# Optimization experiments

Measured on AMD Instinct MI355X. Metric: run time of the kernel, lower is better.

The kernel has to match this reference:

```python
import jax, jax.numpy as jnp
import numpy as np

NEG_INF = -jnp.inf


def _forward(q, k, v, q_indexer, k_indexer, weights, index_topk, end_pos):
    b, h, s, d = q.shape
    scale = float(1.0 / np.sqrt(d))

    # ---- bf16_index: per-head relu(qk) weighted-sum over indexer heads ----
    qi = jnp.swapaxes(q_indexer, 1, 2).astype(jnp.float32)        # [b,hi,s,di]
    ki = jnp.transpose(k_indexer, (0, 2, 3, 1)).astype(jnp.float32)  # [b,hk,di,s] (hk=1 broadcasts)
    p = jax.nn.relu(jnp.matmul(qi, ki))                            # [b,hi,s,s]
    index_score = jnp.einsum('bhqk,bqh->bqk', p, weights.astype(jnp.float32))  # [b,s,s]

    # ---- causal additive mask (attn_mask=None path) ----
    causal = jnp.where(jnp.triu(jnp.ones((s, s), bool), 1), NEG_INF, 0.0).astype(jnp.float32)
    index_score = index_score + causal[None]

    # ---- top-k sparse index selection ----
    K = min(int(index_topk), int(end_pos))
    topk_score, topk_idx = jax.lax.top_k(index_score, K)           # [b,s,K]
    qpos = jnp.arange(s)[None, :, None]
    valid = topk_idx <= qpos
    # invalid slots: torch writes -1 (wraps to last col on CUDA); last col is causally
    # masked for those rows, so dropping the scatter gives an identical final mask.
    scatter_idx = jnp.where(valid, topk_idx, s)
    index_mask = jnp.full((b, s, s), NEG_INF).at[
        jnp.arange(b)[:, None, None], jnp.arange(s)[None, :, None], scatter_idx
    ].set(0.0, mode='drop')

    am = causal[None] + index_mask                                 # [b,s,s]
    masked = jnp.isinf(am) & (am < 0)                              # True = masked out
    keep = ~masked[:, None]                                        # [b,1,s,s]

    # ---- sparse SDPA ----
    scores = jnp.einsum('bhqd,bhkd->bhqk', q, k) * scale
    scores = jnp.where(keep, scores, NEG_INF)
    attn = jax.nn.softmax(scores.astype(jnp.float32), axis=-1)     # [b,h,s,s]
    output = jnp.einsum('bhqk,bhkd->bhqd', attn.astype(q.dtype), v)

    # ---- indexer auxiliary loss (main attn dist uses detached q,k) ----
    main_attn_dist = jax.lax.stop_gradient(attn).sum(axis=1)       # [b,s,s]
    gather_idx = jnp.where(valid, topk_idx, s - 1)                 # -1 wraps to last col
    sel = jnp.take_along_axis(main_attn_dist, gather_idx, axis=-1) # [b,s,K]
    pdist = jax.nn.softmax(topk_score.astype(jnp.float32), axis=-1)
    tgt = sel / jnp.maximum(jnp.sum(jnp.abs(sel), axis=-1, keepdims=True), 1e-12)
    # F.kl_div(log(p+eps), tgt+eps): t*(log t - log p)
    kl = (tgt + 1e-8) * (jnp.log(tgt + 1e-8) - jnp.log(pdist + 1e-8))
    loss = kl.sum(-1).mean()
    return loss, output


def setup_inputs() -> dict:
    key = jax.random.key(0)
    ks = jax.random.split(key, 6)
    b, h, s, d = 1, 16, 2048, 128
    hi, di = 16, 128
    return {
        'q': jax.random.normal(ks[0], (b, h, s, d), jnp.float32),
        'k': jax.random.normal(ks[1], (b, h, s, d), jnp.float32),
        'v': jax.random.normal(ks[2], (b, h, s, d), jnp.float32),
        'q_indexer': jax.random.normal(ks[3], (b, s, hi, di), jnp.float32),
        'k_indexer': jax.random.normal(ks[4], (b, s, 1, di), jnp.float32),
        'weights': jax.random.uniform(ks[5], (b, s, hi), jnp.float32),
        'index_topk': 512,
        'end_pos': 2048,
    }


def reference(q, k, v, q_indexer, k_indexer, weights, index_topk, end_pos):
    return _forward(q, k, v, q_indexer, k_indexer, weights, index_topk, end_pos)
```

## Files before the change

kernel.cpp:

```cpp
#include <hip/hip_runtime.h>
#include <hip/hip_bf16.h>
#include <hip/hip_fp16.h>
#include <math.h>

#define S    2048
#define HQ   16
#define D    128
#define HI   16
#define DI   128
#define KSEL 512
#define OPW  132

typedef __attribute__((ext_vector_type(8))) short short8;
typedef __attribute__((ext_vector_type(4))) float f32x4;
typedef __attribute__((ext_vector_type(2))) float f32x2;
typedef __attribute__((ext_vector_type(2))) _Float16 h2v;

__device__ __forceinline__ float waveReduceSum(float v) {
#pragma unroll
    for (int o = 32; o > 0; o >>= 1) v += __shfl_down(v, o);
    return v;
}
__device__ __forceinline__ float waveReduceMax(float v) {
#pragma unroll
    for (int o = 32; o > 0; o >>= 1) v = fmaxf(v, __shfl_down(v, o));
    return v;
}
__device__ __forceinline__ float blockReduceSum(float v, float* tmp) {
    int wid = threadIdx.x >> 6, lane = threadIdx.x & 63;
    v = waveReduceSum(v);
    __syncthreads();
    if (lane == 0) tmp[wid] = v;
    __syncthreads();
    return tmp[0] + tmp[1] + tmp[2] + tmp[3];
}
__device__ __forceinline__ float blockReduceMax(float v, float* tmp) {
    int wid = threadIdx.x >> 6, lane = threadIdx.x & 63;
    v = waveReduceMax(v);
    __syncthreads();
    if (lane == 0) tmp[wid] = v;
    __syncthreads();
    return fmaxf(fmaxf(tmp[0], tmp[1]), fmaxf(tmp[2], tmp[3]));
}

__device__ __forceinline__ unsigned short f2bf(float f) {
    unsigned int u = __float_as_uint(f);
    return (unsigned short)((u + 0x7FFFu + ((u >> 16) & 1u)) >> 16);
}
__device__ __forceinline__ float bf2f(unsigned short h) {
    return __uint_as_float(((unsigned int)h) << 16);
}
__device__ __forceinline__ float fdot2u(unsigned int a, unsigned int b, float c) {
    return __builtin_amdgcn_fdot2(__builtin_bit_cast(h2v, a),
                                  __builtin_bit_cast(h2v, b), c, false);
}
__device__ __forceinline__ f32x2 f2shfl_xor(f32x2 v, int m) {
    f32x2 r;
    r.x = __shfl_xor(v.x, m);
    r.y = __shfl_xor(v.y, m);
    return r;
}

__global__ __launch_bounds__(256) void f32_to_f16(const float* __restrict__ in,
                                                  unsigned short* __restrict__ outp,
                                                  int n4) {
    for (int i = blockIdx.x * 256 + threadIdx.x; i < n4; i += gridDim.x * 256) {
        float4 x = ((const float4*)in)[i];
        uint2 r;
        r.x = __builtin_bit_cast(unsigned int, __floats2half2_rn(x.x, x.y));
        r.y = __builtin_bit_cast(unsigned int, __floats2half2_rn(x.z, x.w));
        ((uint2*)outp)[i] = r;
    }
}

__global__ __launch_bounds__(256) void f32_to_fp8(const float* __restrict__ in,
                                                  unsigned int* __restrict__ outp,
                                                  int n4) {
    for (int i = blockIdx.x * 256 + threadIdx.x; i < n4; i += gridDim.x * 256) {
        float4 x = ((const float4*)in)[i];
        int u = 0;
        u = __builtin_amdgcn_cvt_pk_fp8_f32(x.x, x.y, u, false);
        u = __builtin_amdgcn_cvt_pk_fp8_f32(x.z, x.w, u, true);
        outp[i] = (unsigned int)u;
    }
}

__global__ __launch_bounds__(256) void split_f32_bf16(const float* __restrict__ in,
                                                      unsigned short* __restrict__ hi,
                                                      unsigned short* __restrict__ lo,
                                                      int n4) {
    for (int i = blockIdx.x * 256 + threadIdx.x; i < n4; i += gridDim.x * 256) {
        float4 x = ((const float4*)in)[i];
        ushort4 h4, l4;
        h4.x = f2bf(x.x); l4.x = f2bf(x.x - bf2f(h4.x));
        h4.y = f2bf(x.y); l4.y = f2bf(x.y - bf2f(h4.y));
        h4.z = f2bf(x.z); l4.z = f2bf(x.z - bf2f(h4.z));
        h4.w = f2bf(x.w); l4.w = f2bf(x.w - bf2f(h4.w));
        ((ushort4*)hi)[i] = h4;
        ((ushort4*)lo)[i] = l4;
    }
}

__device__ void topk_from_scores(const float* scores, int ncand, int K, int q,
                                 int* __restrict__ topk_idx, float* __restrict__ topk_score,
                                 unsigned int* bins, unsigned int* sh_u, unsigned int* cnt_p) {
    const int tid = threadIdx.x;
    if (ncand <= K) {
        for (int j = tid; j < KSEL; j += 256) {
            if (j < ncand) {
                topk_idx[q * KSEL + j]   = j;
                topk_score[q * KSEL + j] = scores[j];
            } else {
                topk_idx[q * KSEL + j]   = -1;
                topk_score[q * KSEL + j] = -INFINITY;
            }
        }
        __syncthreads();
        return;
    }

    unsigned int prefix = 0;
    int need = K;
    for (int pass = 0; pass < 4; ++pass) {
        const int shift = 24 - pass * 8;
        for (int b = tid; b < 256; b += 256) bins[b] = 0;
        __syncthreads();
        const unsigned int himask = (pass == 0) ? 0u : (0xFFFFFFFFu << (shift + 8));
        for (int k = tid; k < ncand; k += 256) {
            unsigned int u = __float_as_uint(scores[k]);
            if ((u & himask) == prefix) atomicAdd(&bins[(u >> shift) & 0xFF], 1u);
        }
        __syncthreads();
        if (tid == 0) {
            int nd = need, b;
            for (b = 255; b >= 1; --b) {
                int c = (int)bins[b];
                if (c >= nd) break;
                nd -= c;
            }
            sh_u[0] = prefix | ((unsigned int)b << shift);
            sh_u[1] = (unsigned int)nd;
        }
        __syncthreads();
        prefix = sh_u[0];
        need   = (int)sh_u[1];
        __syncthreads();
    }
    const unsigned int ueqT = prefix;
    const int count_eq = (int)bins[ueqT & 0xFF];
    __syncthreads();
    if (tid == 0) *cnt_p = 0;
    __syncthreads();

    for (int k = tid; k < ncand; k += 256) {
        unsigned int u = __float_as_uint(scores[k]);
        if (u > ueqT) {
            unsigned int slot = atomicAdd(cnt_p, 1u);
            topk_idx[q * KSEL + slot]   = k;
            topk_score[q * KSEL + slot] = scores[k];
        }
    }
    __syncthreads();
    if (count_eq == need) {
        for (int k = tid; k < ncand; k += 256) {
            if (__float_as_uint(scores[k]) == ueqT) {
                unsigned int slot = atomicAdd(cnt_p, 1u);
                topk_idx[q * KSEL + slot]   = k;
                topk_score[q * KSEL + slot] = __uint_as_float(ueqT);
            }
        }
    } else if (tid == 0) {
        int emitted = 0;
        for (int k = 0; k < ncand && emitted < need; ++k) {
            if (__float_as_uint(scores[k]) == ueqT) {
                unsigned int slot = atomicAdd(cnt_p, 1u);
                topk_idx[q * KSEL + slot]   = k;
                topk_score[q * KSEL + slot] = __uint_as_float(ueqT);
                emitted++;
            }
        }
    }
    __syncthreads();
}

__global__ __launch_bounds__(256) void indexer_mfma(
    const unsigned short* __restrict__ qih, const unsigned short* __restrict__ qil,
    const unsigned short* __restrict__ kih, const unsigned short* __restrict__ kil,
    const float* __restrict__ w,
    const int* __restrict__ topk_p, const int* __restrict__ endpos_p,
    int* __restrict__ topk_idx, float* __restrict__ topk_score)
{
    const int tid  = threadIdx.x;
    const int wv   = tid >> 6;
    const int lane = tid & 63;
    int K = min(topk_p[0], endpos_p[0]);
    K = min(K, KSEL);

    __shared__ float scores[S];
    __shared__ float w_sh[HI];
    __shared__ unsigned int bins[256];
    __shared__ unsigned int sh_u[3];
    __shared__ unsigned int cnt;

    const int mrow = lane & 15;
    const int kgrp = lane >> 4;

    const int b = blockIdx.x;
    for (int qq = 0; qq < 2; ++qq) {
        const int q = qq ? (S - 1 - b) : b;
        if (tid < HI) w_sh[tid] = w[q * HI + tid];
        __syncthreads();

        short8 Ah[4], Al[4];
        {
            const unsigned short* bh = qih + ((size_t)q * HI + mrow) * DI + kgrp * 8;
            const unsigned short* bl = qil + ((size_t)q * HI + mrow) * DI + kgrp * 8;
#pragma unroll
            for (int dc = 0; dc < 4; dc++) {
                Ah[dc] = *(const short8*)(bh + dc * 32);
                Al[dc] = *(const short8*)(bl + dc * 32);
            }
        }
        float wreg[4];
#pragma unroll
        for (int e = 0; e < 4; e++) wreg[e] = w_sh[4 * kgrp + e];

        const int nkt = (q >> 4) + 1;
        for (int t = wv; t < nkt; t += 4) {
            const int k0 = t * 16;
            const unsigned short* bh = kih + ((size_t)(k0 + mrow)) * DI + kgrp * 8;
            const unsigned short* bl = kil + ((size_t)(k0 + mrow)) * DI + kgrp * 8;
            f32x4 acc = {0.f, 0.f, 0.f, 0.f};
#pragma unroll
            for (int dc = 0; dc < 4; dc++) {
                short8 Bh = *(const short8*)(bh + dc * 32);
                short8 Bl = *(const short8*)(bl + dc * 32);
                acc = __builtin_amdgcn_mfma_f32_16x16x32_bf16(Ah[dc], Bh, acc, 0, 0, 0);
                acc = __builtin_amdgcn_mfma_f32_16x16x32_bf16(Ah[dc], Bl, acc, 0, 0, 0);
                acc = __builtin_amdgcn_mfma_f32_16x16x32_bf16(Al[dc], Bh, acc, 0, 0, 0);
            }
            float part = wreg[0] * fmaxf(acc[0], 0.f) + wreg[1] * fmaxf(acc[1], 0.f)
                       + wreg[2] * fmaxf(acc[2], 0.f) + wreg[3] * fmaxf(acc[3], 0.f);
            part += __shfl_xor(part, 16);
            part += __shfl_xor(part, 32);
            if (lane < 16) {
                int k = k0 + lane;
                if (k <= q) scores[k] = part;
            }
        }
        __syncthreads();
        topk_from_scores(scores, q + 1, K, q, topk_idx, topk_score, bins, sh_u, &cnt);
    }
}

__global__ __launch_bounds__(256) void indexer_topk(
    const float* __restrict__ qi,
    const float* __restrict__ ki,
    const float* __restrict__ w,
    const int* __restrict__ topk_p, const int* __restrict__ endpos_p,
    int* __restrict__ topk_idx,
    float* __restrict__ topk_score)
{
    const int q   = blockIdx.x;
    const int tid = threadIdx.x;
    int K = min(topk_p[0], endpos_p[0]);
    K = min(K, KSEL);

    __shared__ float qis[HI * DI];
    __shared__ float wsh[HI];
    __shared__ float scores[S];
    __shared__ unsigned int bins[256];
    __shared__ unsigned int sh_u[3];
    __shared__ unsigned int cnt;

    for (int i = tid; i < HI * DI; i += 256) qis[i] = qi[(size_t)q * HI * DI + i];
    if (tid < HI) wsh[tid] = w[q * HI + tid];
    __syncthreads();

    const int ncand = q + 1;

    for (int kbase = 0; kbase < ncand; kbase += 1024) {
        const int k0 = kbase + tid * 4;
        if (k0 < ncand) {
            float acc[4][HI];
#pragma unroll
            for (int a = 0; a < 4; a++)
#pragma unroll
                for (int h = 0; h < HI; h++) acc[a][h] = 0.f;
            for (int d0 = 0; d0 < DI; d0 += 4) {
                float4 kv[4];
#pragma unroll
                for (int a = 0; a < 4; a++)
                    kv[a] = *(const float4*)&ki[(size_t)(k0 + a) * DI + d0];
#pragma unroll
                for (int h = 0; h < HI; h++) {
                    float4 qv = *(const float4*)&qis[h * DI + d0];
#pragma unroll
                    for (int a = 0; a < 4; a++) {
                        acc[a][h] += qv.x * kv[a].x + qv.y * kv[a].y +
                                     qv.z * kv[a].z + qv.w * kv[a].w;
                    }
                }
            }
#pragma unroll
            for (int a = 0; a < 4; a++) {
                int k = k0 + a;
                if (k < ncand) {
                    float s = 0.f;
#pragma unroll
                    for (int h = 0; h < HI; h++) s += wsh[h] * fmaxf(acc[a][h], 0.f);
                    scores[k] = s;
                }
            }
        }
    }
    __syncthreads();
    topk_from_scores(scores, ncand, K, q, topk_idx, topk_score, bins, sh_u, &cnt);
}

__global__ __launch_bounds__(256) void sparse_attn_v7(
    const float* __restrict__ Q,
    const unsigned short* __restrict__ Kh,
    const unsigned char* __restrict__ Vq,
    const int* __restrict__ topk_idx,
    const int* __restrict__ topk_p, const int* __restrict__ endpos_p,
    float* __restrict__ out,
    float* __restrict__ aacc_g)
{
    const int q   = blockIdx.x;
    const int h   = blockIdx.y;
    const int tid = threadIdx.x;
    int K = min(topk_p[0], endpos_p[0]);
    K = min(K, KSEL);
    const int n = min(q + 1, K);
    const float scale = 0.08838834764831845f;

    __shared__ int          offs[KSEL];
    __shared__ float        sc[KSEL];
    __shared__ unsigned int qh_u[64];
    __shared__ float        opart[16][OPW];
    __shared__ float        tmp[4];

    if (tid < 32) {
        float4 f = ((const float4*)&Q[((size_t)h * S + q) * D])[tid];
        qh_u[2 * tid]     = __builtin_bit_cast(unsigned int,
                              __floats2half2_rn(f.x * scale, f.y * scale));
        qh_u[2 * tid + 1] = __builtin_bit_cast(unsigned int,
                              __floats2half2_rn(f.z * scale, f.w * scale));
    }
    for (int j = tid; j < n; j += 256) offs[j] = topk_idx[q * KSEL + j] << 8;
    __syncthreads();

    const int l8 = tid & 7, grp8 = tid >> 3;
    unsigned int qa[4], qb[4];
#pragma unroll
    for (int c = 0; c < 4; c++) {
        qa[c] = qh_u[l8 * 4 + c];
        qb[c] = qh_u[32 + l8 * 4 + c];
    }
    const char* kbase = (const char*)Kh + (size_t)h * S * 256;
    for (int j = grp8; j < n; j += 32) {
        const char* rb = kbase + offs[j];
        uint4 ra  = *(const uint4*)(rb + l8 * 16);
        uint4 rb2 = *(const uint4*)(rb + 128 + l8 * 16);
        float acc0 = fdot2u(ra.x, qa[0], 0.f);
        float acc1 = fdot2u(rb2.x, qb[0], 0.f);
        acc0 = fdot2u(ra.y, qa[1], acc0);
        acc1 = fdot2u(rb2.y, qb[1], acc1);
        acc0 = fdot2u(ra.z, qa[2], acc0);
        acc1 = fdot2u(rb2.z, qb[2], acc1);
        acc0 = fdot2u(ra.w, qa[3], acc0);
        acc1 = fdot2u(rb2.w, qb[3], acc1);
        float acc = acc0 + acc1;
        acc += __shfl_xor(acc, 1);
        acc += __shfl_xor(acc, 2);
        acc += __shfl_xor(acc, 4);
        if (l8 == 0) sc[j] = acc;
    }
    __syncthreads();

    float lsum = 0.f;
    for (int j = tid; j < n; j += 256) {
        float p = __expf(sc[j]);
        sc[j] = p;
        lsum += p;
    }
    lsum = blockReduceSum(lsum, tmp);
    const float inv = 1.f / lsum;
    for (int j = tid; j < n; j += 256)
        atomicAdd(&aacc_g[(size_t)q * KSEL + j], sc[j] * inv);

    const char* vbase = (const char*)Vq + (size_t)h * S * 128;
    f32x2 o2[8];
#pragma unroll
    for (int i = 0; i < 8; i++) o2[i] = (f32x2){0.f, 0.f};
    for (int j = grp8; j < n; j += 32) {
        const float p = sc[j];
        const f32x2 p2 = {p, p};
        uint4 raw = *(const uint4*)(vbase + (offs[j] >> 1) + l8 * 16);
        o2[0] += p2 * __builtin_amdgcn_cvt_pk_f32_fp8((int)raw.x, false);
        o2[1] += p2 * __builtin_amdgcn_cvt_pk_f32_fp8((int)raw.x, true);
        o2[2] += p2 * __builtin_amdgcn_cvt_pk_f32_fp8((int)raw.y, false);
        o2[3] += p2 * __builtin_amdgcn_cvt_pk_f32_fp8((int)raw.y, true);
        o2[4] += p2 * __builtin_amdgcn_cvt_pk_f32_fp8((int)raw.z, false);
        o2[5] += p2 * __builtin_amdgcn_cvt_pk_f32_fp8((int)raw.z, true);
        o2[6] += p2 * __builtin_amdgcn_cvt_pk_f32_fp8((int)raw.w, false);
        o2[7] += p2 * __builtin_amdgcn_cvt_pk_f32_fp8((int)raw.w, true);
    }
#pragma unroll
    for (int i = 0; i < 8; i++) o2[i] += f2shfl_xor(o2[i], 32);
    const int lane = tid & 63, wvi = tid >> 6;
    if (lane < 32) {
        const int row = wvi * 4 + (lane >> 3);
        float* dst = &opart[row][(lane & 7) * 16];
#pragma unroll
        for (int i = 0; i < 8; i += 2) {
            float4 s;
            s.x = o2[i].x;     s.y = o2[i].y;
            s.z = o2[i + 1].x; s.w = o2[i + 1].y;
            *(float4*)&dst[i * 2] = s;
        }
    }
    __syncthreads();
    if (tid < D) {
        float s = 0.f;
#pragma unroll
        for (int p16 = 0; p16 < 16; ++p16) s += opart[p16][tid];
        out[((size_t)h * S + q) * D + tid] = s * inv;
    }
}

__global__ __launch_bounds__(256) void sparse_attn2(
    const float* __restrict__ Q,
    const float* __restrict__ Km,
    const float* __restrict__ V,
    const int* __restrict__ topk_idx,
    const int* __restrict__ topk_p, const int* __restrict__ endpos_p,
    float* __restrict__ out,
    float* __restrict__ aacc_g)
{
    const int q   = blockIdx.x;
    const int h   = blockIdx.y;
    const int tid = threadIdx.x;
    int K = min(topk_p[0], endpos_p[0]);
    K = min(K, KSEL);
    const int n = min(q + 1, K);
    const float scale = 0.08838834764831845f;

    __shared__ float qvec[D];
    __shared__ int   idxs[KSEL];
    __shared__ float sc[KSEL];
    __shared__ float opart[8][D];
    __shared__ float tmp[4];

    if (tid < 32)
        *(float4*)&qvec[tid * 4] = *(const float4*)&Q[((size_t)h * S + q) * D + tid * 4];
    for (int j = tid; j < n; j += 256) idxs[j] = topk_idx[q * KSEL + j];
    __syncthreads();

    const int l16 = tid & 15, grp = tid >> 4;
    const float4 q1 = *(const float4*)&qvec[l16 * 4];
    const float4 q2 = *(const float4*)&qvec[64 + l16 * 4];
    float lmax = -INFINITY;
    for (int j = grp; j < n; j += 16) {
        const float* kr = &Km[((size_t)h * S + idxs[j]) * D];
        float4 k1 = *(const float4*)&kr[l16 * 4];
        float4 k2 = *(const float4*)&kr[64 + l16 * 4];
        float acc = q1.x * k1.x + q1.y * k1.y + q1.z * k1.z + q1.w * k1.w
                  + q2.x * k2.x + q2.y * k2.y + q2.z * k2.z + q2.w * k2.w;
        acc += __shfl_xor(acc, 1);
        acc += __shfl_xor(acc, 2);
        acc += __shfl_xor(acc, 4);
        acc += __shfl_xor(acc, 8);
        float s = acc * scale;
        if (l16 == 0) sc[j] = s;
        lmax = fmaxf(lmax, s);
    }
    const float m = blockReduceMax(lmax, tmp);

    float lsum = 0.f;
    for (int j = tid; j < n; j += 256) {
        float p = expf(sc[j] - m);
        sc[j] = p;
        lsum += p;
    }
    lsum = blockReduceSum(lsum, tmp);
    const float inv = 1.f / lsum;
    for (int j = tid; j < n; j += 256) {
        float p = sc[j] * inv;
        sc[j] = p;
        atomicAdd(&aacc_g[(size_t)q * KSEL + j], p);
    }
    __syncthreads();

    const int jg = tid >> 5, lD = (tid & 31) * 4;
    float4 o4 = make_float4(0.f, 0.f, 0.f, 0.f);
    for (int j = jg; j < n; j += 8) {
        const float p = sc[j];
        float4 vv = *(const float4*)&V[((size_t)h * S + idxs[j]) * D + lD];
        o4.x += p * vv.x; o4.y += p * vv.y; o4.z += p * vv.z; o4.w += p * vv.w;
    }
    *(float4*)&opart[jg][lD] = o4;
    __syncthreads();
    if (tid < D) {
        float o = 0.f;
#pragma unroll
        for (int p8 = 0; p8 < 8; ++p8) o += opart[p8][tid];
        out[((size_t)h * S + q) * D + tid] = o;
    }
}

__global__ __launch_bounds__(256) void row_loss(
    const float* __restrict__ aacc_g,
    const float* __restrict__ topk_score,
    const int* __restrict__ topk_p, const int* __restrict__ endpos_p,
    float* __restrict__ rowloss)
{
    const int q   = blockIdx.x;
    const int tid = threadIdx.x;
    int K = min(topk_p[0], endpos_p[0]);
    K = min(K, KSEL);
    const int n = min(q + 1, K);

    __shared__ float sc[KSEL];
    __shared__ float aacc[KSEL];
    __shared__ float tmp[4];

    for (int j = tid; j < n; j += 256) aacc[j] = aacc_g[(size_t)q * KSEL + j];

    float tmaxl = -INFINITY;
    for (int j = tid; j < n; j += 256) {
        float t = topk_score[q * KSEL + j];
        sc[j] = t;
        tmaxl = fmaxf(tmaxl, t);
    }
    const float tm = blockReduceMax(tmaxl, tmp);
    float tsum = 0.f;
    for (int j = tid; j < n; j += 256) {
        float e = __expf(sc[j] - tm);
        sc[j] = e;
        tsum += e;
    }
    tsum = blockReduceSum(tsum, tmp);
    const float tinv = 1.f / tsum;

    float sa = 0.f;
    for (int j = tid; j < n; j += 256) sa += fabsf(aacc[j]);
    sa = blockReduceSum(sa, tmp);
    const float denom = fmaxf(sa, 1e-12f);

    float kl = 0.f;
    for (int j = tid; j < n; j += 256) {
        float tgt = aacc[j] / denom + 1e-8f;
        float pd  = sc[j] * tinv + 1e-8f;
        kl += tgt * (logf(tgt) - logf(pd));
    }
    kl = blockReduceSum(kl, tmp);
    if (tid == 0) rowloss[q] = kl;
}

__global__ __launch_bounds__(256) void reduce_loss(const float* __restrict__ rowloss,
                                                   float* __restrict__ out) {
    __shared__ float tmp[4];
    float v = 0.f;
    for (int i = threadIdx.x; i < S; i += 256) v += rowloss[i];
    v = blockReduceSum(v, tmp);
    if (threadIdx.x == 0) out[0] = v / (float)S;
}

extern "C" void kernel_launch(void* const* d_in, const int* in_sizes, int n_in,
                              void* d_out, int out_size, void* d_ws, size_t ws_size,
                              hipStream_t stream) {
    const float* q   = (const float*)d_in[0];
    const float* k   = (const float*)d_in[1];
    const float* v   = (const float*)d_in[2];
    const float* qi  = (const float*)d_in[3];
    const float* ki  = (const float*)d_in[4];
    const float* w   = (const float*)d_in[5];
    const int* topk  = (const int*)d_in[6];
    const int* endp  = (const int*)d_in[7];
    float* out = (float*)d_out;

    char* ws = (char*)d_ws;
    const size_t MB = 1ull << 20;
    int*   topk_idx   = (int*)ws;
    float* topk_score = (float*)(ws + 4 * MB);
    float* aacc_g     = (float*)(ws + 8 * MB);
    float* rowloss    = (float*)(ws + 12 * MB);
    char*  pbuf       = ws + 12 * MB + 65536;
    unsigned short* Kh  = (unsigned short*)pbuf;
    unsigned char*  Vq  = (unsigned char*)(pbuf + 8 * MB);
    unsigned short* qih = (unsigned short*)(pbuf + 12 * MB);
    unsigned short* qil = (unsigned short*)(pbuf + 20 * MB);
    unsigned short* kih = (unsigned short*)(pbuf + 28 * MB);
    unsigned short* kil = (unsigned short*)(pbuf + 28 * MB + 512 * 1024);
    const size_t need_attn = 12 * MB + 65536 + 12 * MB;
    const size_t need_idx  = 12 * MB + 65536 + 29 * MB;

    if (ws_size >= need_idx) {
        hipLaunchKernelGGL(split_f32_bf16, dim3(2048), dim3(256), 0, stream,
                           qi, qih, qil, S * HI * DI / 4);
        hipLaunchKernelGGL(split_f32_bf16, dim3(256), dim3(256), 0, stream,
                           ki, kih, kil, S * DI / 4);
        hipLaunchKernelGGL(indexer_mfma, dim3(S / 2), dim3(256), 0, stream,
                           qih, qil, kih, kil, w, topk, endp, topk_idx, topk_score);
    } else {
        hipLaunchKernelGGL(indexer_topk, dim3(S), dim3(256), 0, stream,
                           qi, ki, w, topk, endp, topk_idx, topk_score);
    }

    hipMemsetAsync(aacc_g, 0, (size_t)S * KSEL * sizeof(float), stream);

    if (ws_size >= need_attn) {
        const int n4 = HQ * S * D / 4;
        hipLaunchKernelGGL(f32_to_f16, dim3(2048), dim3(256), 0, stream, k, Kh, n4);
        hipLaunchKernelGGL(f32_to_fp8, dim3(2048), dim3(256), 0, stream, v,
                           (unsigned int*)Vq, n4);
        hipLaunchKernelGGL(sparse_attn_v7, dim3(S, HQ), dim3(256), 0, stream,
                           q, Kh, Vq, topk_idx, topk, endp, out + 1, aacc_g);
    } else {
        hipLaunchKernelGGL(sparse_attn2, dim3(S, HQ), dim3(256), 0, stream,
                           q, k, v, topk_idx, topk, endp, out + 1, aacc_g);
    }

    hipLaunchKernelGGL(row_loss, dim3(S), dim3(256), 0, stream,
                       aacc_g, topk_score, topk, endp, rowloss);
    hipLaunchKernelGGL(reduce_loss, dim3(1), dim3(256), 0, stream,
                       rowloss, out);
}
```

Baseline: 446.9 us.

## Fuse conversion kernels, parallelize radix-select bin scan, use fast log

Merges the two K/V conversion kernels into one launch and the two indexer split kernels into one launch, cutting launch overhead and inter-kernel gaps. Replaces the serial single-thread 256-bin threshold search in the top-k radix select with a 64-lane wave suffix-scan, shortening the critical path on every pass. Switches logf to __logf in the KL loss, trading a little accuracy for speed. The wave scan's boundary handling is more intricate, so tie and edge cases could behave differently from the serial loop.

```diff
diff --git a/kernel.cpp b/kernel.cpp
--- a/kernel.cpp
+++ b/kernel.cpp
@@ -61,44 +61,47 @@
     return r;
 }
 
-__global__ __launch_bounds__(256) void f32_to_f16(const float* __restrict__ in,
-                                                  unsigned short* __restrict__ outp,
+__global__ __launch_bounds__(256) void convert_kv(const float* __restrict__ kin,
+                                                  const float* __restrict__ vin,
+                                                  unsigned short* __restrict__ Kh,
+                                                  unsigned int* __restrict__ Vq,
                                                   int n4) {
-    for (int i = blockIdx.x * 256 + threadIdx.x; i < n4; i += gridDim.x * 256) {
-        float4 x = ((const float4*)in)[i];
+    const int stride = gridDim.x * 256;
+    for (int i = blockIdx.x * 256 + threadIdx.x; i < n4; i += stride) {
+        float4 x = ((const float4*)kin)[i];
         uint2 r;
         r.x = __builtin_bit_cast(unsigned int, __floats2half2_rn(x.x, x.y));
         r.y = __builtin_bit_cast(unsigned int, __floats2half2_rn(x.z, x.w));
-        ((uint2*)outp)[i] = r;
-    }
-}
-
-__global__ __launch_bounds__(256) void f32_to_fp8(const float* __restrict__ in,
-                                                  unsigned int* __restrict__ outp,
-                                                  int n4) {
-    for (int i = blockIdx.x * 256 + threadIdx.x; i < n4; i += gridDim.x * 256) {
-        float4 x = ((const float4*)in)[i];
+        ((uint2*)Kh)[i] = r;
+        float4 y = ((const float4*)vin)[i];
         int u = 0;
-        u = __builtin_amdgcn_cvt_pk_fp8_f32(x.x, x.y, u, false);
-        u = __builtin_amdgcn_cvt_pk_fp8_f32(x.z, x.w, u, true);
-        outp[i] = (unsigned int)u;
-    }
-}
-
-__global__ __launch_bounds__(256) void split_f32_bf16(const float* __restrict__ in,
-                                                      unsigned short* __restrict__ hi,
-                                                      unsigned short* __restrict__ lo,
-                                                      int n4) {
-    for (int i = blockIdx.x * 256 + threadIdx.x; i < n4; i += gridDim.x * 256) {
-        float4 x = ((const float4*)in)[i];
-        ushort4 h4, l4;
-        h4.x = f2bf(x.x); l4.x = f2bf(x.x - bf2f(h4.x));
-        h4.y = f2bf(x.y); l4.y = f2bf(x.y - bf2f(h4.y));
-        h4.z = f2bf(x.z); l4.z = f2bf(x.z - bf2f(h4.z));
-        h4.w = f2bf(x.w); l4.w = f2bf(x.w - bf2f(h4.w));
-        ((ushort4*)hi)[i] = h4;
-        ((ushort4*)lo)[i] = l4;
-    }
+        u = __builtin_amdgcn_cvt_pk_fp8_f32(y.x, y.y, u, false);
+        u = __builtin_amdgcn_cvt_pk_fp8_f32(y.z, y.w, u, true);
+        Vq[i] = (unsigned int)u;
+    }
+}
+
+__device__ __forceinline__ void split4(const float* in, unsigned short* hi,
+                                       unsigned short* lo, int i) {
+    float4 x = ((const float4*)in)[i];
+    ushort4 h4, l4;
+    h4.x = f2bf(x.x); l4.x = f2bf(x.x - bf2f(h4.x));
+    h4.y = f2bf(x.y); l4.y = f2bf(x.y - bf2f(h4.y));
+    h4.z = f2bf(x.z); l4.z = f2bf(x.z - bf2f(h4.z));
+    h4.w = f2bf(x.w); l4.w = f2bf(x.w - bf2f(h4.w));
+    ((ushort4*)hi)[i] = h4;
+    ((ushort4*)lo)[i] = l4;
+}
+__global__ __launch_bounds__(256) void split_qiki(
+    const float* __restrict__ qi, unsigned short* __restrict__ qih,
+    unsigned short* __restrict__ qil,
+    const float* __restrict__ ki, unsigned short* __restrict__ kih,
+    unsigned short* __restrict__ kil, int n4q, int n4k) {
+    const int stride = gridDim.x * 256;
+    for (int i = blockIdx.x * 256 + threadIdx.x; i < n4q; i += stride)
+        split4(qi, qih, qil, i);
+    for (int i = blockIdx.x * 256 + threadIdx.x; i < n4k; i += stride)
+        split4(ki, kih, kil, i);
 }
 
 __device__ void topk_from_scores(const float* scores, int ncand, int K, int q,
@@ -131,15 +134,41 @@
             if ((u & himask) == prefix) atomicAdd(&bins[(u >> shift) & 0xFF], 1u);
         }
         __syncthreads();
-        if (tid == 0) {
-            int nd = need, b;
-            for (b = 255; b >= 1; --b) {
-                int c = (int)bins[b];
-                if (c >= nd) break;
-                nd -= c;
-            }
-            sh_u[0] = prefix | ((unsigned int)b << shift);
-            sh_u[1] = (unsigned int)nd;
+        if (tid < 64) {
+            const int l = tid;
+            unsigned int b0 = bins[4 * l], b1 = bins[4 * l + 1],
+                         b2 = bins[4 * l + 2], b3 = bins[4 * l + 3];
+            unsigned int s3 = b3, s2 = b2 + s3, s1 = b1 + s2, s0 = b0 + s1;
+            unsigned int acc = s0;
+#pragma unroll
+            for (int off = 1; off < 64; off <<= 1) {
+                unsigned int t = __shfl_down(acc, off);
+                if (l + off < 64) acc += t;
+            }
+            const unsigned int above = acc - s0;
+            const unsigned int S0 = s0 + above, S1 = s1 + above,
+                               S2 = s2 + above, S3 = s3 + above;
+            const unsigned int nd = (unsigned int)need;
+            if (4 * l + 0 >= 1 && S0 >= nd && S1 < nd) {
+                sh_u[0] = prefix | ((unsigned int)(4 * l + 0) << shift);
+                sh_u[1] = nd - S1;
+            }
+            if (S1 >= nd && S2 < nd) {
+                sh_u[0] = prefix | ((unsigned int)(4 * l + 1) << shift);
+                sh_u[1] = nd - S2;
+            }
+            if (S2 >= nd && S3 < nd) {
+                sh_u[0] = prefix | ((unsigned int)(4 * l + 2) << shift);
+                sh_u[1] = nd - S3;
+            }
+            if (S3 >= nd && above < nd) {
+                sh_u[0] = prefix | ((unsigned int)(4 * l + 3) << shift);
+                sh_u[1] = nd - above;
+            }
+            if (l == 0 && S1 < nd) {
+                sh_u[0] = prefix;
+                sh_u[1] = nd - S1;
+            }
         }
         __syncthreads();
         prefix = sh_u[0];
@@ -553,7 +582,7 @@
     for (int j = tid; j < n; j += 256) {
         float tgt = aacc[j] / denom + 1e-8f;
         float pd  = sc[j] * tinv + 1e-8f;
-        kl += tgt * (logf(tgt) - logf(pd));
+        kl += tgt * (__logf(tgt) - __logf(pd));
     }
     kl = blockReduceSum(kl, tmp);
     if (tid == 0) rowloss[q] = kl;
@@ -598,10 +627,9 @@
     const size_t need_idx  = 12 * MB + 65536 + 29 * MB;
 
     if (ws_size >= need_idx) {
-        hipLaunchKernelGGL(split_f32_bf16, dim3(2048), dim3(256), 0, stream,
-                           qi, qih, qil, S * HI * DI / 4);
-        hipLaunchKernelGGL(split_f32_bf16, dim3(256), dim3(256), 0, stream,
-                           ki, kih, kil, S * DI / 4);
+        hipLaunchKernelGGL(split_qiki, dim3(2048), dim3(256), 0, stream,
+                           qi, qih, qil, ki, kih, kil,
+                           S * HI * DI / 4, S * DI / 4);
         hipLaunchKernelGGL(indexer_mfma, dim3(S / 2), dim3(256), 0, stream,
                            qih, qil, kih, kil, w, topk, endp, topk_idx, topk_score);
     } else {
@@ -613,9 +641,8 @@
 
     if (ws_size >= need_attn) {
         const int n4 = HQ * S * D / 4;
-        hipLaunchKernelGGL(f32_to_f16, dim3(2048), dim3(256), 0, stream, k, Kh, n4);
-        hipLaunchKernelGGL(f32_to_fp8, dim3(2048), dim3(256), 0, stream, v,
-                           (unsigned int*)Vq, n4);
+        hipLaunchKernelGGL(convert_kv, dim3(2048), dim3(256), 0, stream,
+                           k, v, Kh, (unsigned int*)Vq, n4);
         hipLaunchKernelGGL(sparse_attn_v7, dim3(S, HQ), dim3(256), 0, stream,
                            q, Kh, Vq, topk_idx, topk, endp, out + 1, aacc_g);
     } else {
```

New measurement: 400.4 us. 10.4% less time.
